# Optimization experiments

Measured on AMD Instinct MI355X. Metric: run time of the kernel, lower is better.

The kernel has to match this reference:

```python
import jax, jax.numpy as jnp
import numpy as np

NUM_HEADS = 8
LN_EPS = 1e-5

def setup_inputs() -> dict:
    key = jax.random.key(0)
    ks = jax.random.split(key, 8)
    B, C, H, W = 2, 512, 64, 64
    dim = C
    s = 1.0 / np.sqrt(dim)
    return {
        "pet_feat": jax.random.normal(ks[0], (B, C, H, W), jnp.float32),
        "ct_feat": jax.random.normal(ks[1], (B, C, H, W), jnp.float32),
        "Wq": jax.random.normal(ks[2], (dim, dim), jnp.float32) * s,
        "Wk": jax.random.normal(ks[3], (dim, dim), jnp.float32) * s,
        "Wv": jax.random.normal(ks[4], (dim, dim), jnp.float32) * s,
        "Wp": jax.random.normal(ks[5], (dim, dim), jnp.float32) * s,
        "bp": jnp.zeros((dim,), jnp.float32),
        "gamma": jnp.ones((dim,), jnp.float32),
        "beta": jnp.zeros((dim,), jnp.float32),
    }

def reference(pet_feat, ct_feat, Wq, Wk, Wv, Wp, bp, gamma, beta):
    B, C, H, W = pet_feat.shape
    L = H * W
    nh = NUM_HEADS
    hd = C // nh
    scale = hd ** (-0.5)
    # b c h w -> b (h w) c
    pet_seq = pet_feat.reshape(B, C, L).transpose(0, 2, 1)
    ct_seq = ct_feat.reshape(B, C, L).transpose(0, 2, 1)
    # linear projections (torch Linear: x @ W.T), split heads: b l (h d) -> b h l d
    q = (pet_seq @ Wq.T).reshape(B, L, nh, hd).transpose(0, 2, 1, 3)
    k = (ct_seq @ Wk.T).reshape(B, L, nh, hd).transpose(0, 2, 1, 3)
    v = (ct_seq @ Wv.T).reshape(B, L, nh, hd).transpose(0, 2, 1, 3)
    attn = jnp.einsum('bhld,bhmd->bhlm', q, k) * scale
    attn = jax.nn.softmax(attn, axis=-1)
    x = jnp.einsum('bhlm,bhmd->bhld', attn, v)
    # b h l d -> b l (h d)
    x = x.transpose(0, 2, 1, 3).reshape(B, L, C)
    x = x @ Wp.T + bp
    x = pet_seq + x
    # LayerNorm over channel dim
    mu = jnp.mean(x, axis=-1, keepdims=True)
    var = jnp.mean(jnp.square(x - mu), axis=-1, keepdims=True)
    x = (x - mu) * jax.lax.rsqrt(var + LN_EPS) * gamma + beta
    # b (h w) c -> b c h w
    return x.transpose(0, 2, 1).reshape(B, C, H, W)
```

## Files before the change

kernel.cpp:

```cpp
#include <hip/hip_runtime.h>

#define B_ 2
#define C_ 512
#define L_ 4096
#define NH 8
#define HD 64

typedef short bf16x8 __attribute__((ext_vector_type(8)));
typedef float f32x4 __attribute__((ext_vector_type(4)));
typedef unsigned short u16;
typedef unsigned short u16x8 __attribute__((ext_vector_type(8)));

static __device__ __forceinline__ u16 f2bf(float f) {
    union { float f; unsigned u; } v; v.f = f;
    unsigned u = v.u;
    u += 0x7fff + ((u >> 16) & 1);
    return (u16)(u >> 16);
}

static __device__ __forceinline__ float bf2f(u16 h) {
    union { unsigned u; float f; } v; v.u = ((unsigned)h) << 16;
    return v.f;
}

static __device__ __forceinline__ unsigned cvtpk(float lo, float hi) {
    unsigned r;
    asm("v_cvt_pk_bf16_f32 %0, %1, %2" : "=v"(r) : "v"(lo), "v"(hi));
    return r;
}

__global__ __launch_bounds__(256) void transpose_conv_kernel(
        const float* __restrict__ pet, const float* __restrict__ ct,
        u16* __restrict__ petT, u16* __restrict__ ctT) {
    __shared__ float tile[64][65];
    int z  = blockIdx.z;
    int b  = z >> 1;
    const float* src = (z & 1) ? ct : pet;
    u16* dst         = (z & 1) ? ctT : petT;
    int c0 = blockIdx.y * 64;
    int l0 = blockIdx.x * 64;
    int t  = threadIdx.x;
    int i  = t >> 2;
    int jc = (t & 3) * 16;
    const float* sp = src + ((size_t)(b * C_ + c0 + i)) * L_ + l0 + jc;
#pragma unroll
    for (int p = 0; p < 4; ++p) {
        float4 v = *(const float4*)(sp + p * 4);
        tile[i][jc + p * 4 + 0] = v.x;
        tile[i][jc + p * 4 + 1] = v.y;
        tile[i][jc + p * 4 + 2] = v.z;
        tile[i][jc + p * 4 + 3] = v.w;
    }
    __syncthreads();
    int cc = (t & 3) * 16;
    u16* dp = dst + ((size_t)(b * L_ + l0 + i)) * C_ + c0 + cc;
    u16x8 o0, o1;
#pragma unroll
    for (int q = 0; q < 8; ++q) o0[q] = f2bf(tile[cc + q][i]);
#pragma unroll
    for (int q = 0; q < 8; ++q) o1[q] = f2bf(tile[cc + 8 + q][i]);
    *(u16x8*)(dp)     = o0;
    *(u16x8*)(dp + 8) = o1;
}

__global__ __launch_bounds__(256) void f2bf4_kernel(
        const float* __restrict__ s0, const float* __restrict__ s1,
        const float* __restrict__ s2, const float* __restrict__ s3,
        u16* __restrict__ d0, u16* __restrict__ d1,
        u16* __restrict__ d2, u16* __restrict__ d3) {
    const int n = 512 * 512;
    int idx = blockIdx.x * blockDim.x + threadIdx.x;
    int stride = gridDim.x * blockDim.x;
    for (int i = idx; i < n; i += stride) {
        d0[i] = f2bf(s0[i]);
        d1[i] = f2bf(s1[i]);
        d2[i] = f2bf(s2[i]);
        d3[i] = f2bf(s3[i]);
    }
}

__global__ __launch_bounds__(256) void gemm_nt_kernel(
        const u16* __restrict__ A, const u16* __restrict__ Bt,
        u16* __restrict__ Cm, int M, int N, int K,
        size_t aZ, size_t btZ, size_t cZ) {
    __shared__ u16 Al[64][72];
    __shared__ u16 Bl[64][72];
    A  += (size_t)blockIdx.z * aZ;
    Bt += (size_t)blockIdx.z * btZ;
    Cm += (size_t)blockIdx.z * cZ;
    int m0 = blockIdx.x * 64;
    int n0 = blockIdx.y * 64;
    int t = threadIdx.x;
    int w = t >> 6, lane = t & 63, ll = lane & 15, lh = lane >> 4;
    int moff = (w & 1) * 32, noff = (w >> 1) * 32;
    f32x4 acc[2][2] = {};
    int srow  = t >> 2;
    int skoff = (t & 3) * 16;
    const u16* Ap = A  + (size_t)(m0 + srow) * K + skoff;
    const u16* Bp = Bt + (size_t)(n0 + srow) * K + skoff;
    for (int kb = 0; kb < K; kb += 64) {
        u16x8 a0 = *(const u16x8*)(Ap + kb);
        u16x8 a1 = *(const u16x8*)(Ap + kb + 8);
        u16x8 b0 = *(const u16x8*)(Bp + kb);
        u16x8 b1 = *(const u16x8*)(Bp + kb + 8);
        *(u16x8*)&Al[srow][skoff]     = a0;
        *(u16x8*)&Al[srow][skoff + 8] = a1;
        *(u16x8*)&Bl[srow][skoff]     = b0;
        *(u16x8*)&Bl[srow][skoff + 8] = b1;
        __syncthreads();
#pragma unroll
        for (int kc = 0; kc < 2; ++kc) {
            bf16x8 af[2], bfr[2];
#pragma unroll
            for (int mf = 0; mf < 2; ++mf)
                af[mf] = *(const bf16x8*)&Al[moff + mf * 16 + ll][kc * 32 + lh * 8];
#pragma unroll
            for (int nf = 0; nf < 2; ++nf)
                bfr[nf] = *(const bf16x8*)&Bl[noff + nf * 16 + ll][kc * 32 + lh * 8];
#pragma unroll
            for (int mf = 0; mf < 2; ++mf)
#pragma unroll
                for (int nf = 0; nf < 2; ++nf)
                    acc[mf][nf] = __builtin_amdgcn_mfma_f32_16x16x32_bf16(
                        af[mf], bfr[nf], acc[mf][nf], 0, 0, 0);
        }
        __syncthreads();
    }
#pragma unroll
    for (int mf = 0; mf < 2; ++mf)
#pragma unroll
        for (int nf = 0; nf < 2; ++nf)
#pragma unroll
            for (int r = 0; r < 4; ++r) {
                int row = m0 + moff + mf * 16 + lh * 4 + r;
                int col = n0 + noff + nf * 16 + ll;
                Cm[(size_t)row * N + col] = f2bf(acc[mf][nf][r]);
            }
}

__global__ __launch_bounds__(256) void attn_kernel(
        const u16* __restrict__ q, const u16* __restrict__ k,
        const u16* __restrict__ vt, u16* __restrict__ Xp,
        float* __restrict__ lp) {
    __shared__ u16 Kl[2][64][76];
    __shared__ u16 Vl[2][64][72];
    int l0 = blockIdx.x * 128;
    int h  = blockIdx.y;
    int z  = blockIdx.z;
    int b  = z >> 1;
    int split = z & 1;
    int t = threadIdx.x;
    int w = t >> 6, lane = t & 63, ll = lane & 15, lh = lane >> 4;
    const float C1 = 0.125f * 1.44269504088896340736f;
    const float M0 = 16.0f;
    const int NT = L_ / 64;
    const int t0 = split * (NT / 2);
    const size_t NE = (size_t)B_ * L_ * C_;

    bf16x8 qf[2][2];
#pragma unroll
    for (int u = 0; u < 2; ++u) {
        const u16* qp = q + ((size_t)(b * L_ + l0 + w * 32 + u * 16 + ll)) * C_
                          + h * HD + lh * 8;
        qf[u][0] = *(const bf16x8*)qp;
        qf[u][1] = *(const bf16x8*)(qp + 32);
    }
    int krow[4];
#pragma unroll
    for (int nf = 0; nf < 4; ++nf)
        krow[nf] = 32 * (nf & 1) + 4 * (nf >> 1) + 8 * (ll >> 2) + (ll & 3);

    int srow = t >> 2;
    int soff = (t & 3) * 16;
    const u16* kp = k  + ((size_t)(b * L_ + t0 * 64 + srow)) * C_ + h * HD + soff;
    const u16* vp = vt + ((size_t)(b * C_ + h * HD + srow)) * L_ + t0 * 64 + soff;

    u16x8 ka0 = *(const u16x8*)(kp);
    u16x8 ka1 = *(const u16x8*)(kp + 8);
    u16x8 va0 = *(const u16x8*)(vp);
    u16x8 va1 = *(const u16x8*)(vp + 8);
    *(u16x8*)&Kl[0][srow][soff]     = ka0;
    *(u16x8*)&Kl[0][srow][soff + 8] = ka1;
    *(u16x8*)&Vl[0][srow][soff]     = va0;
    *(u16x8*)&Vl[0][srow][soff + 8] = va1;
    kp += (size_t)64 * C_;
    vp += 64;

    f32x4 o[4][2] = {};
    float l_run[2] = {0.f, 0.f};

    int cur = 0;
    const int NLOC = NT / 2;
    for (int tile = 0; tile < NLOC; ++tile) {
        __syncthreads();
        const bool pre = (tile < NLOC - 1);
        if (pre) {
            ka0 = *(const u16x8*)(kp);
            ka1 = *(const u16x8*)(kp + 8);
            va0 = *(const u16x8*)(vp);
            va1 = *(const u16x8*)(vp + 8);
            kp += (size_t)64 * C_;
            vp += 64;
        }
        bf16x8 kf[4][2], vf[4][2];
#pragma unroll
        for (int nf = 0; nf < 4; ++nf) {
            kf[nf][0] = *(const bf16x8*)&Kl[cur][krow[nf]][lh * 8];
            kf[nf][1] = *(const bf16x8*)&Kl[cur][krow[nf]][32 + lh * 8];
        }
#pragma unroll
        for (int df = 0; df < 4; ++df) {
            vf[df][0] = *(const bf16x8*)&Vl[cur][df * 16 + ll][lh * 8];
            vf[df][1] = *(const bf16x8*)&Vl[cur][df * 16 + ll][32 + lh * 8];
        }

        f32x4 s[2][4] = {};
#pragma unroll
        for (int kc = 0; kc < 2; ++kc)
#pragma unroll
            for (int nf = 0; nf < 4; ++nf)
#pragma unroll
                for (int u = 0; u < 2; ++u)
                    s[u][nf] = __builtin_amdgcn_mfma_f32_16x16x32_bf16(
                        kf[nf][kc], qf[u][kc], s[u][nf], 0, 0, 0);

        union { unsigned uu[4]; bf16x8 v; } pb[2][2];
#pragma unroll
        for (int u = 0; u < 2; ++u) {
            float ts = 0.f;
#pragma unroll
            for (int nf = 0; nf < 4; ++nf)
#pragma unroll
                for (int r = 0; r < 4; ++r) {
                    float pv = __builtin_amdgcn_exp2f(fmaf(s[u][nf][r], C1, -M0));
                    s[u][nf][r] = pv;
                    ts += pv;
                }
            l_run[u] += ts;
#pragma unroll
            for (int kc = 0; kc < 2; ++kc) {
                pb[kc][u].uu[0] = cvtpk(s[u][kc][0],     s[u][kc][1]);
                pb[kc][u].uu[1] = cvtpk(s[u][kc][2],     s[u][kc][3]);
                pb[kc][u].uu[2] = cvtpk(s[u][kc + 2][0], s[u][kc + 2][1]);
                pb[kc][u].uu[3] = cvtpk(s[u][kc + 2][2], s[u][kc + 2][3]);
            }
        }
#pragma unroll
        for (int kc = 0; kc < 2; ++kc)
#pragma unroll
            for (int df = 0; df < 4; ++df)
#pragma unroll
                for (int u = 0; u < 2; ++u)
                    o[df][u] = __builtin_amdgcn_mfma_f32_16x16x32_bf16(
                        vf[df][kc], pb[kc][u].v, o[df][u], 0, 0, 0);

        if (pre) {
            int nxt = cur ^ 1;
            *(u16x8*)&Kl[nxt][srow][soff]     = ka0;
            *(u16x8*)&Kl[nxt][srow][soff + 8] = ka1;
            *(u16x8*)&Vl[nxt][srow][soff]     = va0;
            *(u16x8*)&Vl[nxt][srow][soff + 8] = va1;
            cur = nxt;
        }
    }

#pragma unroll
    for (int u = 0; u < 2; ++u) {
        l_run[u] += __shfl_xor(l_run[u], 16, 64);
        l_run[u] += __shfl_xor(l_run[u], 32, 64);
    }
    u16* Xs = Xp + (size_t)split * NE;
#pragma unroll
    for (int u = 0; u < 2; ++u) {
        int row = l0 + w * 32 + u * 16 + ll;
        if (lh == 0)
            lp[((size_t)(split * B_ + b) * NH + h) * L_ + row] = l_run[u];
        u16* xp = Xs + ((size_t)(b * L_ + row)) * C_ + h * HD + 4 * lh;
#pragma unroll
        for (int df = 0; df < 4; ++df) {
            union { unsigned uu[2]; } pk;
            pk.uu[0] = cvtpk(o[df][u][0], o[df][u][1]);
            pk.uu[1] = cvtpk(o[df][u][2], o[df][u][3]);
            *(uint2*)(xp + df * 16) = *(uint2*)pk.uu;
        }
    }
}

__global__ __launch_bounds__(256) void outln_kernel(
        const u16* __restrict__ X, const u16* __restrict__ Wpb,
        const float* __restrict__ bp, const float* __restrict__ gamma,
        const float* __restrict__ beta, const float* __restrict__ pet,
        const float* __restrict__ lp, float* __restrict__ out) {
    __shared__ u16 Al[16][520];
    __shared__ float red[16][4][2];
    const size_t NE  = (size_t)B_ * L_ * C_;
    const size_t NLP = (size_t)B_ * NH * L_;
    int g0 = blockIdx.x * 16;
    int b  = g0 >> 12;
    int l0 = g0 & (L_ - 1);
    int t = threadIdx.x;
    int w = t >> 6, lane = t & 63, ll = lane & 15, lh = lane >> 4;
    {
        int row  = t >> 4;
        int koff = (t & 15) * 32;
        int h    = koff >> 6;
        int labs = l0 + row;
        float lsum = lp[((size_t)b * NH + h) * L_ + labs]
                   + lp[NLP + ((size_t)b * NH + h) * L_ + labs];
        float linv = 1.f / lsum;
        const u16* x1 = X +      ((size_t)(g0 + row)) * C_ + koff;
        const u16* x2 = X + NE + ((size_t)(g0 + row)) * C_ + koff;
#pragma unroll
        for (int p = 0; p < 4; ++p) {
            u16x8 v1 = *(const u16x8*)(x1 + p * 8);
            u16x8 v2 = *(const u16x8*)(x2 + p * 8);
            u16x8 o8;
#pragma unroll
            for (int j = 0; j < 8; ++j)
                o8[j] = f2bf((bf2f(v1[j]) + bf2f(v2[j])) * linv);
            *(u16x8*)&Al[row][koff + p * 8] = o8;
        }
    }
    __syncthreads();
    int nbase = w * 128;
    f32x4 acc[8] = {};
    for (int kc = 0; kc < 16; ++kc) {
        bf16x8 af = *(const bf16x8*)&Al[ll][kc * 32 + lh * 8];
#pragma unroll
        for (int nf = 0; nf < 8; ++nf) {
            int c = nbase + nf * 16 + ll;
            bf16x8 bfr = *(const bf16x8*)(Wpb + (size_t)c * C_ + kc * 32 + lh * 8);
            acc[nf] = __builtin_amdgcn_mfma_f32_16x16x32_bf16(af, bfr, acc[nf], 0, 0, 0);
        }
    }
    float psum[4] = {}, psq[4] = {};
#pragma unroll
    for (int nf = 0; nf < 8; ++nf) {
        int c = nbase + nf * 16 + ll;
        float bias = bp[c];
#pragma unroll
        for (int r = 0; r < 4; ++r) {
            int l = l0 + lh * 4 + r;
            float v = acc[nf][r] + bias + pet[((size_t)(b * C_ + c)) * L_ + l];
            acc[nf][r] = v;
            psum[r] += v;
            psq[r]  += v * v;
        }
    }
#pragma unroll
    for (int x = 1; x < 16; x <<= 1)
#pragma unroll
        for (int r = 0; r < 4; ++r) {
            psum[r] += __shfl_xor(psum[r], x, 64);
            psq[r]  += __shfl_xor(psq[r], x, 64);
        }
    if (ll == 0) {
#pragma unroll
        for (int r = 0; r < 4; ++r) {
            red[lh * 4 + r][w][0] = psum[r];
            red[lh * 4 + r][w][1] = psq[r];
        }
    }
    __syncthreads();
#pragma unroll
    for (int r = 0; r < 4; ++r) {
        int row = lh * 4 + r;
        float s  = red[row][0][0] + red[row][1][0] + red[row][2][0] + red[row][3][0];
        float sq = red[row][0][1] + red[row][1][1] + red[row][2][1] + red[row][3][1];
        float mean = s * (1.f / 512.f);
        float var  = sq * (1.f / 512.f) - mean * mean;
        float rs = rsqrtf(var + 1e-5f);
        int l = l0 + row;
#pragma unroll
        for (int nf = 0; nf < 8; ++nf) {
            int c = nbase + nf * 16 + ll;
            float v = (acc[nf][r] - mean) * rs * gamma[c] + beta[c];
            out[((size_t)(b * C_ + c)) * L_ + l] = v;
        }
    }
}

extern "C" void kernel_launch(void* const* d_in, const int* in_sizes, int n_in,
                              void* d_out, int out_size, void* d_ws, size_t ws_size,
                              hipStream_t stream) {
    const float* pet   = (const float*)d_in[0];
    const float* ct    = (const float*)d_in[1];
    const float* Wq    = (const float*)d_in[2];
    const float* Wk    = (const float*)d_in[3];
    const float* Wv    = (const float*)d_in[4];
    const float* Wp    = (const float*)d_in[5];
    const float* bp    = (const float*)d_in[6];
    const float* gamma = (const float*)d_in[7];
    const float* beta  = (const float*)d_in[8];
    float* out = (float*)d_out;

    char* ws = (char*)d_ws;
    const size_t SZ  = (size_t)B_ * L_ * C_ * 2;
    const size_t NE  = (size_t)B_ * L_ * C_;
    const size_t WSZ = (size_t)512 * 512;
    u16* petT = (u16*)(ws);
    u16* ctT  = (u16*)(ws + SZ);
    u16* qb   = (u16*)(ws + 2 * SZ);
    u16* kb   = (u16*)(ws + 3 * SZ);
    u16* vtb  = (u16*)(ws + 4 * SZ);
    u16* wqb  = (u16*)(ws + 5 * SZ);
    u16* wkb  = wqb + WSZ;
    u16* wvb  = wkb + WSZ;
    u16* wpb  = wvb + WSZ;
    float* lpb = (float*)(ws + 5 * SZ + 4 * WSZ * 2);
    u16* X2   = (u16*)((char*)lpb + 2ull * B_ * NH * L_ * 4);
    (void)kb;

    dim3 tb(256);
    transpose_conv_kernel<<<dim3(L_ / 64, C_ / 64, 2 * B_), tb, 0, stream>>>(
        pet, ct, petT, ctT);
    f2bf4_kernel<<<dim3(256), tb, 0, stream>>>(Wq, Wk, Wv, Wp, wqb, wkb, wvb, wpb);

    gemm_nt_kernel<<<dim3((B_ * L_) / 64, C_ / 64, 2), tb, 0, stream>>>(
        petT, wqb, qb, B_ * L_, C_, C_,
        NE, WSZ, NE);
    gemm_nt_kernel<<<dim3(C_ / 64, L_ / 64, B_), tb, 0, stream>>>(
        wvb, ctT, vtb, C_, L_, C_,
        0, (size_t)L_ * C_, (size_t)C_ * L_);

    u16* X1 = petT;
    (void)X2;
    attn_kernel<<<dim3(L_ / 128, NH, 2 * B_), tb, 0, stream>>>(
        qb, kb, vtb, X1, lpb);

    outln_kernel<<<dim3((B_ * L_) / 16), tb, 0, stream>>>(
        X1, wpb, bp, gamma, beta, pet, lpb, out);
}
```

Measured before the change: 179.2 us.

## Double-buffer GEMM shared tiles and single-buffer attention K/V staging

The GEMM kernel now keeps two LDS buffers and prefetches the next K-slice into registers while the MFMAs run on the current one, which removes one barrier per iteration. The attention kernel goes the other way: it drops its double buffer and loads K/V synchronously with two barriers per tile. That halves its LDS use, which could allow more resident blocks, but the load latency is no longer hidden behind compute. Since attention dominates the runtime, the net effect is uncertain.

```diff
diff --git a/kernel.cpp b/kernel.cpp
--- a/kernel.cpp
+++ b/kernel.cpp
@@ -83,8 +83,8 @@
         const u16* __restrict__ A, const u16* __restrict__ Bt,
         u16* __restrict__ Cm, int M, int N, int K,
         size_t aZ, size_t btZ, size_t cZ) {
-    __shared__ u16 Al[64][72];
-    __shared__ u16 Bl[64][72];
+    __shared__ u16 Al[2][64][72];
+    __shared__ u16 Bl[2][64][72];
     A  += (size_t)blockIdx.z * aZ;
     Bt += (size_t)blockIdx.z * btZ;
     Cm += (size_t)blockIdx.z * cZ;
@@ -98,25 +98,38 @@
     int skoff = (t & 3) * 16;
     const u16* Ap = A  + (size_t)(m0 + srow) * K + skoff;
     const u16* Bp = Bt + (size_t)(n0 + srow) * K + skoff;
-    for (int kb = 0; kb < K; kb += 64) {
-        u16x8 a0 = *(const u16x8*)(Ap + kb);
-        u16x8 a1 = *(const u16x8*)(Ap + kb + 8);
-        u16x8 b0 = *(const u16x8*)(Bp + kb);
-        u16x8 b1 = *(const u16x8*)(Bp + kb + 8);
-        *(u16x8*)&Al[srow][skoff]     = a0;
-        *(u16x8*)&Al[srow][skoff + 8] = a1;
-        *(u16x8*)&Bl[srow][skoff]     = b0;
-        *(u16x8*)&Bl[srow][skoff + 8] = b1;
+
+    u16x8 a0 = *(const u16x8*)(Ap);
+    u16x8 a1 = *(const u16x8*)(Ap + 8);
+    u16x8 b0 = *(const u16x8*)(Bp);
+    u16x8 b1 = *(const u16x8*)(Bp + 8);
+    *(u16x8*)&Al[0][srow][skoff]     = a0;
+    *(u16x8*)&Al[0][srow][skoff + 8] = a1;
+    *(u16x8*)&Bl[0][srow][skoff]     = b0;
+    *(u16x8*)&Bl[0][srow][skoff + 8] = b1;
+    Ap += 64; Bp += 64;
+
+    int cur = 0;
+    const int NKB = K / 64;
+    for (int kb = 0; kb < NKB; ++kb) {
         __syncthreads();
+        const bool pre = (kb < NKB - 1);
+        if (pre) {
+            a0 = *(const u16x8*)(Ap);
+            a1 = *(const u16x8*)(Ap + 8);
+            b0 = *(const u16x8*)(Bp);
+            b1 = *(const u16x8*)(Bp + 8);
+            Ap += 64; Bp += 64;
+        }
 #pragma unroll
         for (int kc = 0; kc < 2; ++kc) {
             bf16x8 af[2], bfr[2];
 #pragma unroll
             for (int mf = 0; mf < 2; ++mf)
-                af[mf] = *(const bf16x8*)&Al[moff + mf * 16 + ll][kc * 32 + lh * 8];
+                af[mf] = *(const bf16x8*)&Al[cur][moff + mf * 16 + ll][kc * 32 + lh * 8];
 #pragma unroll
             for (int nf = 0; nf < 2; ++nf)
-                bfr[nf] = *(const bf16x8*)&Bl[noff + nf * 16 + ll][kc * 32 + lh * 8];
+                bfr[nf] = *(const bf16x8*)&Bl[cur][noff + nf * 16 + ll][kc * 32 + lh * 8];
 #pragma unroll
             for (int mf = 0; mf < 2; ++mf)
 #pragma unroll
@@ -124,7 +137,14 @@
                     acc[mf][nf] = __builtin_amdgcn_mfma_f32_16x16x32_bf16(
                         af[mf], bfr[nf], acc[mf][nf], 0, 0, 0);
         }
-        __syncthreads();
+        if (pre) {
+            int nxt = cur ^ 1;
+            *(u16x8*)&Al[nxt][srow][skoff]     = a0;
+            *(u16x8*)&Al[nxt][srow][skoff + 8] = a1;
+            *(u16x8*)&Bl[nxt][srow][skoff]     = b0;
+            *(u16x8*)&Bl[nxt][srow][skoff + 8] = b1;
+            cur = nxt;
+        }
     }
 #pragma unroll
     for (int mf = 0; mf < 2; ++mf)
@@ -142,8 +162,8 @@
         const u16* __restrict__ q, const u16* __restrict__ k,
         const u16* __restrict__ vt, u16* __restrict__ Xp,
         float* __restrict__ lp) {
-    __shared__ u16 Kl[2][64][76];
-    __shared__ u16 Vl[2][64][72];
+    __shared__ u16 Kl[64][76];
+    __shared__ u16 Vl[64][72];
     int l0 = blockIdx.x * 128;
     int h  = blockIdx.y;
     int z  = blockIdx.z;
@@ -154,7 +174,8 @@
     const float C1 = 0.125f * 1.44269504088896340736f;
     const float M0 = 16.0f;
     const int NT = L_ / 64;
-    const int t0 = split * (NT / 2);
+    const int NLOC = NT / 2;
+    const int t0 = split * NLOC;
     const size_t NE = (size_t)B_ * L_ * C_;
 
     bf16x8 qf[2][2];
@@ -175,43 +196,30 @@
     const u16* kp = k  + ((size_t)(b * L_ + t0 * 64 + srow)) * C_ + h * HD + soff;
     const u16* vp = vt + ((size_t)(b * C_ + h * HD + srow)) * L_ + t0 * 64 + soff;
 
-    u16x8 ka0 = *(const u16x8*)(kp);
-    u16x8 ka1 = *(const u16x8*)(kp + 8);
-    u16x8 va0 = *(const u16x8*)(vp);
-    u16x8 va1 = *(const u16x8*)(vp + 8);
-    *(u16x8*)&Kl[0][srow][soff]     = ka0;
-    *(u16x8*)&Kl[0][srow][soff + 8] = ka1;
-    *(u16x8*)&Vl[0][srow][soff]     = va0;
-    *(u16x8*)&Vl[0][srow][soff + 8] = va1;
-    kp += (size_t)64 * C_;
-    vp += 64;
-
     f32x4 o[4][2] = {};
     float l_run[2] = {0.f, 0.f};
 
-    int cur = 0;
-    const int NLOC = NT / 2;
     for (int tile = 0; tile < NLOC; ++tile) {
+        u16x8 ka0 = *(const u16x8*)(kp);
+        u16x8 ka1 = *(const u16x8*)(kp + 8);
+        u16x8 va0 = *(const u16x8*)(vp);
+        u16x8 va1 = *(const u16x8*)(vp + 8);
+        *(u16x8*)&Kl[srow][soff]     = ka0;
+        *(u16x8*)&Kl[srow][soff + 8] = ka1;
+        *(u16x8*)&Vl[srow][soff]     = va0;
+        *(u16x8*)&Vl[srow][soff + 8] = va1;
         __syncthreads();
-        const bool pre = (tile < NLOC - 1);
-        if (pre) {
-            ka0 = *(const u16x8*)(kp);
-            ka1 = *(const u16x8*)(kp + 8);
-            va0 = *(const u16x8*)(vp);
-            va1 = *(const u16x8*)(vp + 8);
-            kp += (size_t)64 * C_;
-            vp += 64;
-        }
+
         bf16x8 kf[4][2], vf[4][2];
 #pragma unroll
         for (int nf = 0; nf < 4; ++nf) {
-            kf[nf][0] = *(const bf16x8*)&Kl[cur][krow[nf]][lh * 8];
-            kf[nf][1] = *(const bf16x8*)&Kl[cur][krow[nf]][32 + lh * 8];
+            kf[nf][0] = *(const bf16x8*)&Kl[krow[nf]][lh * 8];
+            kf[nf][1] = *(const bf16x8*)&Kl[krow[nf]][32 + lh * 8];
         }
 #pragma unroll
         for (int df = 0; df < 4; ++df) {
-            vf[df][0] = *(const bf16x8*)&Vl[cur][df * 16 + ll][lh * 8];
-            vf[df][1] = *(const bf16x8*)&Vl[cur][df * 16 + ll][32 + lh * 8];
+            vf[df][0] = *(const bf16x8*)&Vl[df * 16 + ll][lh * 8];
+            vf[df][1] = *(const bf16x8*)&Vl[df * 16 + ll][32 + lh * 8];
         }
 
         f32x4 s[2][4] = {};
@@ -253,15 +261,9 @@
                 for (int u = 0; u < 2; ++u)
                     o[df][u] = __builtin_amdgcn_mfma_f32_16x16x32_bf16(
                         vf[df][kc], pb[kc][u].v, o[df][u], 0, 0, 0);
-
-        if (pre) {
-            int nxt = cur ^ 1;
-            *(u16x8*)&Kl[nxt][srow][soff]     = ka0;
-            *(u16x8*)&Kl[nxt][srow][soff + 8] = ka1;
-            *(u16x8*)&Vl[nxt][srow][soff]     = va0;
-            *(u16x8*)&Vl[nxt][srow][soff + 8] = va1;
-            cur = nxt;
-        }
+        __syncthreads();
+        kp += (size_t)64 * C_;
+        vp += 64;
     }
 
 #pragma unroll
@@ -408,7 +410,6 @@
     u16* wvb  = wkb + WSZ;
     u16* wpb  = wvb + WSZ;
     float* lpb = (float*)(ws + 5 * SZ + 4 * WSZ * 2);
-    u16* X2   = (u16*)((char*)lpb + 2ull * B_ * NH * L_ * 4);
     (void)kb;
 
     dim3 tb(256);
@@ -424,7 +425,6 @@
         0, (size_t)L_ * C_, (size_t)C_ * L_);
 
     u16* X1 = petT;
-    (void)X2;
     attn_kernel<<<dim3(L_ / 128, NH, 2 * B_), tb, 0, stream>>>(
         qb, kb, vtb, X1, lpb);
 
```

After: 187.5 us. 1.05x slower.

## Fold softmax scale into Q, seed scores with offset, compute row sums via MFMA

Applied to the files above, without the earlier changes.

Pre-multiplies the bf16 Q fragments by the log2-scaled softmax factor so the per-element fma before exp2 disappears. The score accumulators start at -M0 so the MFMA output feeds exp2 directly. The running row sum of P is now produced by an extra MFMA against a vector of ones instead of scalar adds and cross-lane shuffles. Together these cut VALU work in the softmax inner loop. In exchange each step adds MFMA work, and rounding the scaled Q back to bf16 changes precision.

```diff
diff --git a/kernel.cpp b/kernel.cpp
--- a/kernel.cpp
+++ b/kernel.cpp
@@ -154,7 +154,8 @@
     const float C1 = 0.125f * 1.44269504088896340736f;
     const float M0 = 16.0f;
     const int NT = L_ / 64;
-    const int t0 = split * (NT / 2);
+    const int NLOC = NT / 2;
+    const int t0 = split * NLOC;
     const size_t NE = (size_t)B_ * L_ * C_;
 
     bf16x8 qf[2][2];
@@ -164,7 +165,21 @@
                           + h * HD + lh * 8;
         qf[u][0] = *(const bf16x8*)qp;
         qf[u][1] = *(const bf16x8*)(qp + 32);
-    }
+#pragma unroll
+        for (int kc = 0; kc < 2; ++kc) {
+            union { bf16x8 v; u16x8 s; unsigned uu[4]; } io;
+            io.v = qf[u][kc];
+#pragma unroll
+            for (int j = 0; j < 4; ++j)
+                io.uu[j] = cvtpk(bf2f(io.s[2 * j]) * C1,
+                                 bf2f(io.s[2 * j + 1]) * C1);
+            qf[u][kc] = io.v;
+        }
+    }
+    union { unsigned uu[4]; bf16x8 v; } onesf;
+#pragma unroll
+    for (int j = 0; j < 4; ++j) onesf.uu[j] = 0x3F803F80u;
+
     int krow[4];
 #pragma unroll
     for (int nf = 0; nf < 4; ++nf)
@@ -187,10 +202,10 @@
     vp += 64;
 
     f32x4 o[4][2] = {};
-    float l_run[2] = {0.f, 0.f};
+    f32x4 lacc[2] = {};
+    const f32x4 sinit = {-M0, -M0, -M0, -M0};
 
     int cur = 0;
-    const int NLOC = NT / 2;
     for (int tile = 0; tile < NLOC; ++tile) {
         __syncthreads();
         const bool pre = (tile < NLOC - 1);
@@ -214,7 +229,11 @@
             vf[df][1] = *(const bf16x8*)&Vl[cur][df * 16 + ll][32 + lh * 8];
         }
 
-        f32x4 s[2][4] = {};
+        f32x4 s[2][4];
+#pragma unroll
+        for (int u = 0; u < 2; ++u)
+#pragma unroll
+            for (int nf = 0; nf < 4; ++nf) s[u][nf] = sinit;
 #pragma unroll
         for (int kc = 0; kc < 2; ++kc)
 #pragma unroll
@@ -227,16 +246,11 @@
         union { unsigned uu[4]; bf16x8 v; } pb[2][2];
 #pragma unroll
         for (int u = 0; u < 2; ++u) {
-            float ts = 0.f;
 #pragma unroll
             for (int nf = 0; nf < 4; ++nf)
 #pragma unroll
-                for (int r = 0; r < 4; ++r) {
-                    float pv = __builtin_amdgcn_exp2f(fmaf(s[u][nf][r], C1, -M0));
-                    s[u][nf][r] = pv;
-                    ts += pv;
-                }
-            l_run[u] += ts;
+                for (int r = 0; r < 4; ++r)
+                    s[u][nf][r] = __builtin_amdgcn_exp2f(s[u][nf][r]);
 #pragma unroll
             for (int kc = 0; kc < 2; ++kc) {
                 pb[kc][u].uu[0] = cvtpk(s[u][kc][0],     s[u][kc][1]);
@@ -248,11 +262,14 @@
 #pragma unroll
         for (int kc = 0; kc < 2; ++kc)
 #pragma unroll
-            for (int df = 0; df < 4; ++df)
-#pragma unroll
-                for (int u = 0; u < 2; ++u)
+            for (int u = 0; u < 2; ++u) {
+#pragma unroll
+                for (int df = 0; df < 4; ++df)
                     o[df][u] = __builtin_amdgcn_mfma_f32_16x16x32_bf16(
                         vf[df][kc], pb[kc][u].v, o[df][u], 0, 0, 0);
+                lacc[u] = __builtin_amdgcn_mfma_f32_16x16x32_bf16(
+                    onesf.v, pb[kc][u].v, lacc[u], 0, 0, 0);
+            }
 
         if (pre) {
             int nxt = cur ^ 1;
@@ -264,17 +281,12 @@
         }
     }
 
-#pragma unroll
-    for (int u = 0; u < 2; ++u) {
-        l_run[u] += __shfl_xor(l_run[u], 16, 64);
-        l_run[u] += __shfl_xor(l_run[u], 32, 64);
-    }
     u16* Xs = Xp + (size_t)split * NE;
 #pragma unroll
     for (int u = 0; u < 2; ++u) {
         int row = l0 + w * 32 + u * 16 + ll;
         if (lh == 0)
-            lp[((size_t)(split * B_ + b) * NH + h) * L_ + row] = l_run[u];
+            lp[((size_t)(split * B_ + b) * NH + h) * L_ + row] = lacc[u][0];
         u16* xp = Xs + ((size_t)(b * L_ + row)) * C_ + h * HD + 4 * lh;
 #pragma unroll
         for (int df = 0; df < 4; ++df) {
@@ -408,7 +420,6 @@
     u16* wvb  = wkb + WSZ;
     u16* wpb  = wvb + WSZ;
     float* lpb = (float*)(ws + 5 * SZ + 4 * WSZ * 2);
-    u16* X2   = (u16*)((char*)lpb + 2ull * B_ * NH * L_ * 4);
     (void)kb;
 
     dim3 tb(256);
@@ -424,7 +435,6 @@
         0, (size_t)L_ * C_, (size_t)C_ * L_);
 
     u16* X1 = petT;
-    (void)X2;
     attn_kernel<<<dim3(L_ / 128, NH, 2 * B_), tb, 0, stream>>>(
         qb, kb, vtb, X1, lpb);
 
```

Result: faster. 170.8 us (-4.7%).
